# Kernel optimization log

Measured on AMD Instinct MI355X. Metric: run time of the kernel, lower is better.

## Reference

```python
import jax, jax.numpy as jnp
import numpy as np

D_MODEL = 256
NUM_HEADS = 8
HEAD_DIM = D_MODEL // NUM_HEADS


def setup_inputs() -> dict:
    key = jax.random.key(0)
    ks = jax.random.split(key, 16)
    B, C, H, W = 2, D_MODEL, 64, 64
    s = 0.02
    inp = {
        "query_feat": jax.random.normal(ks[0], (B, C, H, W), jnp.float32),
        "lateral_feat": jax.random.normal(ks[1], (B, C, H, W), jnp.float32),
        # 1x1 convs == per-pixel linear layers: weight (out, in), bias (out,)
        "Wq": jax.random.normal(ks[2], (C, C), jnp.float32) * s,
        "bq": jnp.zeros((C,), jnp.float32),
        "Wk": jax.random.normal(ks[3], (C, C), jnp.float32) * s,
        "bk": jnp.zeros((C,), jnp.float32),
        "Wv": jax.random.normal(ks[4], (C, C), jnp.float32) * s,
        "bv": jnp.zeros((C,), jnp.float32),
        "Wo": jax.random.normal(ks[5], (C, C), jnp.float32) * s,
        "bo": jnp.zeros((C,), jnp.float32),
        "W1": jax.random.normal(ks[6], (4 * C, C), jnp.float32) * s,
        "b1": jnp.zeros((4 * C,), jnp.float32),
        "W2": jax.random.normal(ks[7], (C, 4 * C), jnp.float32) * s,
        "b2": jnp.zeros((C,), jnp.float32),
    }
    return inp


def reference(query_feat, lateral_feat, Wq, bq, Wk, bk, Wv, bv, Wo, bo, W1, b1, W2, b2):
    B, C, H, W = query_feat.shape
    N = H * W
    h, d = NUM_HEADS, HEAD_DIM
    scale = d ** -0.5

    # (B,C,H,W) -> (B,N,C) tokens
    xq = query_feat.reshape(B, C, N).transpose(0, 2, 1)
    xl = lateral_feat.reshape(B, C, N).transpose(0, 2, 1)

    # 1x1-conv projections = dense per-token linear
    Q = (xq @ Wq.T + bq).reshape(B, N, h, d).transpose(0, 2, 1, 3)  # (B,h,N,d)
    K = (xl @ Wk.T + bk).reshape(B, N, h, d).transpose(0, 2, 1, 3)
    V = (xl @ Wv.T + bv).reshape(B, N, h, d).transpose(0, 2, 1, 3)

    scores = jnp.einsum("bhqd,bhkd->bhqk", Q, K) * scale  # (B,h,N,N)
    attn = jax.nn.softmax(scores, axis=-1)  # dropout = identity at inference
    out = jnp.einsum("bhqk,bhkd->bhqd", attn, V)  # (B,h,N,d)

    out = out.transpose(0, 2, 1, 3).reshape(B, N, C)  # (B,N,C)
    out = out @ Wo.T + bo
    out = out.transpose(0, 2, 1).reshape(B, C, H, W)
    out = out + query_feat  # residual

    # MLP on channels (1x1 convs + exact GELU)
    t = out.reshape(B, C, N).transpose(0, 2, 1)  # (B,N,C)
    hdn = jax.nn.gelu(t @ W1.T + b1, approximate=False)  # (B,N,4C)
    mlp = (hdn @ W2.T + b2).transpose(0, 2, 1).reshape(B, C, H, W)
    return out + mlp
```

## Files before the change

### kernel.cpp

```cpp
#include <hip/hip_runtime.h>
#include <math.h>

namespace {

constexpr int kB  = 2;
constexpr int kC  = 256;
constexpr int kN  = 4096;
constexpr int kHD = 32;
constexpr int kC4 = 1024;

typedef __attribute__((ext_vector_type(8))) short bf16x8;
typedef __attribute__((ext_vector_type(4))) float f32x4;
typedef __attribute__((ext_vector_type(16))) float f32x16;

__device__ __forceinline__ float gelu_exact(float x) {
  return 0.5f * x * (1.0f + erff(x * 0.70710678118654752f));
}

__device__ __forceinline__ unsigned short f2bf(float x) {
  unsigned u = __builtin_bit_cast(unsigned, x);
  u += 0x7FFFu + ((u >> 16) & 1u);
  return (unsigned short)(u >> 16);
}

__device__ __forceinline__ float bf2f(unsigned short us) {
  return __builtin_bit_cast(float, (unsigned)us << 16);
}

__device__ __forceinline__ float exp2_hw(float x) {
#if __has_builtin(__builtin_amdgcn_exp2f)
  return __builtin_amdgcn_exp2f(x);
#else
  float r;
  asm("v_exp_f32 %0, %1\n\ts_nop 1" : "=v"(r) : "v"(x));
  return r;
#endif
}

__device__ __forceinline__ unsigned cvt_pk_bf16(float lo, float hi) {
  unsigned r;
  asm("v_cvt_pk_bf16_f32 %0, %1, %2" : "=v"(r) : "v"(lo), "v"(hi));
  return r;
}

__global__ __launch_bounds__(256)
void convert_all(const float* __restrict__ qfeat, const float* __restrict__ lfeat,
                 const float* __restrict__ Wq, const float* __restrict__ Wk,
                 const float* __restrict__ Wv, const float* __restrict__ Wo,
                 const float* __restrict__ W1, const float* __restrict__ W2,
                 unsigned short* __restrict__ qtok, unsigned short* __restrict__ ltok,
                 unsigned short* __restrict__ wbf)
{
  __shared__ float Lds[32][36];
  const int z = blockIdx.z;
  const int t = threadIdx.x;
  if (z < 4) {
    const float* src = (z < kB) ? qfeat : lfeat;
    unsigned short* dst = (z < kB) ? qtok : ltok;
    const int b = z & 1;
    src += (size_t)b * kC * kN;
    dst += (size_t)b * kN * kC;
    const int n0 = blockIdx.x * 32, c0 = blockIdx.y * 32;
    const int r = t >> 3, q4 = (t & 7) * 4;
    {
      const float4 v = *(const float4*)&src[(size_t)(c0 + r) * kN + n0 + q4];
      Lds[r][q4 + 0] = v.x; Lds[r][q4 + 1] = v.y; Lds[r][q4 + 2] = v.z; Lds[r][q4 + 3] = v.w;
    }
    __syncthreads();
    ushort4 p;
    p.x = f2bf(Lds[q4 + 0][r]); p.y = f2bf(Lds[q4 + 1][r]);
    p.z = f2bf(Lds[q4 + 2][r]); p.w = f2bf(Lds[q4 + 3][r]);
    *(ushort4*)&dst[(size_t)(n0 + r) * kC + c0 + q4] = p;
  } else {
    const int wi = blockIdx.y * 128 + blockIdx.x;
    if (wi >= 768) return;
    const int i4 = wi * 1024 + t * 4;
    const float* s; int base;
    if      (i4 < 65536)  { s = Wq; base = 0; }
    else if (i4 < 131072) { s = Wk; base = 65536; }
    else if (i4 < 196608) { s = Wv; base = 131072; }
    else if (i4 < 262144) { s = Wo; base = 196608; }
    else if (i4 < 524288) { s = W1; base = 262144; }
    else                  { s = W2; base = 524288; }
    const float4 v = *(const float4*)&s[i4 - base];
    ushort4 p;
    p.x = f2bf(v.x); p.y = f2bf(v.y); p.z = f2bf(v.z); p.w = f2bf(v.w);
    *(ushort4*)&wbf[i4] = p;
  }
}

template <int EPI, bool GELU, bool RES>
__global__ __launch_bounds__(256)
void gemm_mfma(const unsigned short* __restrict__ Wbf,
               const unsigned short* __restrict__ Xtok,
               const float* __restrict__ bias, const float* __restrict__ res,
               void* __restrict__ Y1, void* __restrict__ Y2,
               int M, int Nn, int K, float oscale)
{
  __shared__ unsigned short Wlds[64 * 64];
  __shared__ unsigned short Xlds[64 * 64];

  const int z = blockIdx.z;
  Xtok += (size_t)z * Nn * K;

  const int t = threadIdx.x;
  const int w = t >> 6, l = t & 63;
  const int r = l & 15, g = l >> 4;
  const int wm = w >> 1, wn = w & 1;
  const int m0 = blockIdx.y * 64, n0 = blockIdx.x * 64;

  const int rw = t >> 3;
  const int sw = (t & 7) ^ (rw & 7);
  const unsigned short* wsrc = Wbf + (size_t)(m0 + rw) * K + sw * 8;
  const unsigned short* xsrc = Xtok + (size_t)(n0 + rw) * K + sw * 8;

  f32x4 acc[2][2];
#pragma unroll
  for (int i = 0; i < 2; ++i)
#pragma unroll
    for (int j = 0; j < 2; ++j) acc[i][j] = {0.f, 0.f, 0.f, 0.f};

  bf16x8 wrg[2], xrg[2];
#pragma unroll
  for (int j = 0; j < 2; ++j) {
    wrg[j] = *(const bf16x8*)(wsrc + (size_t)(32 * j) * K);
    xrg[j] = *(const bf16x8*)(xsrc + (size_t)(32 * j) * K);
  }

  for (int k0 = 0; k0 < K; k0 += 64) {
    __syncthreads();
    *(bf16x8*)((char*)Wlds + t * 16)         = wrg[0];
    *(bf16x8*)((char*)Wlds + (256 + t) * 16) = wrg[1];
    *(bf16x8*)((char*)Xlds + t * 16)         = xrg[0];
    *(bf16x8*)((char*)Xlds + (256 + t) * 16) = xrg[1];
    __syncthreads();
    if (k0 + 64 < K) {
#pragma unroll
      for (int j = 0; j < 2; ++j) {
        wrg[j] = *(const bf16x8*)(wsrc + (size_t)(32 * j) * K + k0 + 64);
        xrg[j] = *(const bf16x8*)(xsrc + (size_t)(32 * j) * K + k0 + 64);
      }
    }
#pragma unroll
    for (int kc = 0; kc < 2; ++kc) {
      const int sl = ((kc * 4 + g) ^ (r & 7)) * 16;
      bf16x8 a0 = *(const bf16x8*)((const char*)Wlds + (wm * 32 + r) * 128 + sl);
      bf16x8 a1 = *(const bf16x8*)((const char*)Wlds + (wm * 32 + 16 + r) * 128 + sl);
      bf16x8 b0 = *(const bf16x8*)((const char*)Xlds + (wn * 32 + r) * 128 + sl);
      bf16x8 b1 = *(const bf16x8*)((const char*)Xlds + (wn * 32 + 16 + r) * 128 + sl);
      acc[0][0] = __builtin_amdgcn_mfma_f32_16x16x32_bf16(a0, b0, acc[0][0], 0, 0, 0);
      acc[0][1] = __builtin_amdgcn_mfma_f32_16x16x32_bf16(a0, b1, acc[0][1], 0, 0, 0);
      acc[1][0] = __builtin_amdgcn_mfma_f32_16x16x32_bf16(a1, b0, acc[1][0], 0, 0, 0);
      acc[1][1] = __builtin_amdgcn_mfma_f32_16x16x32_bf16(a1, b1, acc[1][1], 0, 0, 0);
    }
  }

#pragma unroll
  for (int f = 0; f < 2; ++f) {
    const int mb = m0 + wm * 32 + f * 16 + 4 * g;
    const float* bp = bias + mb;
    if constexpr (EPI == 4) { if (mb >= (M >> 1)) bp = res + (mb - (M >> 1)); }
    const float4 b4 = *(const float4*)bp;
#pragma unroll
    for (int fn = 0; fn < 2; ++fn) {
      const int n = n0 + wn * 32 + fn * 16 + r;
      float v[4];
      v[0] = (acc[f][fn][0] + b4.x) * oscale; v[1] = (acc[f][fn][1] + b4.y) * oscale;
      v[2] = (acc[f][fn][2] + b4.z) * oscale; v[3] = (acc[f][fn][3] + b4.w) * oscale;
      if (GELU) {
#pragma unroll
        for (int q = 0; q < 4; ++q) v[q] = gelu_exact(v[q]);
      }
      if (RES) {
#pragma unroll
        for (int q = 0; q < 4; ++q)
          v[q] += res[(size_t)z * M * Nn + (size_t)(mb + q) * Nn + n];
      }
      if constexpr (EPI == 1) {
        unsigned short* Yt = (unsigned short*)Y1 + (size_t)z * Nn * M;
        ushort4 pk;
        pk.x = f2bf(v[0]); pk.y = f2bf(v[1]); pk.z = f2bf(v[2]); pk.w = f2bf(v[3]);
        *(ushort4*)&Yt[(size_t)n * M + mb] = pk;
      }
      if constexpr (EPI == 4) {
        const int Mh = M >> 1;
        if (mb < Mh) {
          unsigned short* Yt = (unsigned short*)Y1 + (size_t)z * Nn * Mh;
          ushort4 pk;
          pk.x = f2bf(v[0]); pk.y = f2bf(v[1]); pk.z = f2bf(v[2]); pk.w = f2bf(v[3]);
          *(ushort4*)&Yt[(size_t)n * Mh + mb] = pk;
        } else {
          unsigned short* Yc = (unsigned short*)Y2 + (size_t)z * Mh * Nn;
#pragma unroll
          for (int q = 0; q < 4; ++q) Yc[(size_t)(mb - Mh + q) * Nn + n] = f2bf(v[q]);
        }
      }
      if constexpr (EPI == 6) {
        float* Yf = (float*)Y1 + (size_t)z * M * Nn;
        const unsigned short* Rt = (const unsigned short*)Y2 + (size_t)z * Nn * M;
#pragma unroll
        for (int q = 0; q < 4; ++q)
          Yf[(size_t)(mb + q) * Nn + n] = v[q] + bf2f(Rt[(size_t)n * M + mb + q]);
      }
    }
  }
}

__global__ __launch_bounds__(512, 4)
void attn_mfma32(const unsigned short* __restrict__ Qbf,
                 const unsigned short* __restrict__ Kbf,
                 const unsigned short* __restrict__ Vbf,
                 unsigned short* __restrict__ Aout)
{
  __shared__ char smem[32768];

  const int id = blockIdx.x;
  const int bh = id & 15;
  const int b = bh >> 3, hd = bh & 7;
  const int t = threadIdx.x;
  const int w = t >> 6, l = t & 63;
  const int r = l & 31, hi = l >> 5;
  const int qg = w >> 2, kh = w & 3;

  const unsigned short* Qb = Qbf + (size_t)b * kN * kC;
  const unsigned short* Kb = Kbf + (size_t)b * kN * kC;
  const unsigned short* Vb = Vbf + ((size_t)b * kC + hd * kHD) * kN;
  unsigned short* Ap = Aout + (size_t)b * kN * kC;

  const int q0 = (id >> 4) * 64 + qg * 32;

  const bf16x8 qf0 = *(const bf16x8*)&Qb[(size_t)(q0 + r) * kC + hd * kHD + hi * 8];
  const bf16x8 qf1 = *(const bf16x8*)&Qb[(size_t)(q0 + r) * kC + hd * kHD + 16 + hi * 8];

  const int tq = t & 127, qd = t >> 7;
  const int skey = tq >> 1, schalf = (tq & 1) * 2;
  const int sd = tq >> 2, scp = (tq & 3) * 2;
  const unsigned short* ksrc = Kb + (size_t)(qd * 1024 + skey) * kC + hd * kHD + schalf * 8;
  const unsigned short* vsrc = Vb + (size_t)sd * kN + qd * 1024 + scp * 8;
  char* kdst0 = smem + qd * 8192 + ((schalf)*64 + (skey ^ (9 * schalf))) * 16;
  char* kdst1 = smem + qd * 8192 + ((schalf + 1) * 64 + (skey ^ (9 * (schalf + 1)))) * 16;
  char* vdst0 = smem + qd * 8192 + 4096 + ((scp)*32 + (sd ^ scp)) * 16;
  char* vdst1 = smem + qd * 8192 + 4096 + ((scp + 1) * 32 + (sd ^ (scp + 1))) * 16;

  const int kb0 = kh * 8192;
  int koff[2][2], voff[2][2];
#pragma unroll
  for (int ds = 0; ds < 2; ++ds)
#pragma unroll
    for (int tile = 0; tile < 2; ++tile) {
      const int c = 2 * ds + hi;
      koff[ds][tile] = kb0 + (c * 64 + tile * 32 + (r ^ (9 * c))) * 16;
    }
#pragma unroll
  for (int ktile = 0; ktile < 2; ++ktile)
#pragma unroll
    for (int kc = 0; kc < 2; ++kc) {
      const int c = ktile * 4 + kc * 2 + hi;
      voff[ktile][kc] = kb0 + 4096 + (c * 32 + (r ^ c)) * 16;
    }

  const f32x16 ZV = {0.f};
  f32x16 oA = ZV, oB = ZV;
  float lsum = 0.f;

  bf16x8 krg0 = *(const bf16x8*)ksrc, krg1 = *(const bf16x8*)(ksrc + 8);
  bf16x8 vrg0 = *(const bf16x8*)vsrc, vrg1 = *(const bf16x8*)(vsrc + 8);

  for (int it = 0; it < 16; ++it) {
    __syncthreads();
    *(bf16x8*)kdst0 = krg0; *(bf16x8*)kdst1 = krg1;
    *(bf16x8*)vdst0 = vrg0; *(bf16x8*)vdst1 = vrg1;
    __syncthreads();
    if (it + 1 < 16) {
      ksrc += (size_t)64 * kC; vsrc += 64;
      krg0 = *(const bf16x8*)ksrc; krg1 = *(const bf16x8*)(ksrc + 8);
      vrg0 = *(const bf16x8*)vsrc; vrg1 = *(const bf16x8*)(vsrc + 8);
    }

    bf16x8 ka00 = *(const bf16x8*)(smem + koff[0][0]);
    bf16x8 ka10 = *(const bf16x8*)(smem + koff[1][0]);
    bf16x8 ka01 = *(const bf16x8*)(smem + koff[0][1]);
    bf16x8 ka11 = *(const bf16x8*)(smem + koff[1][1]);
    __builtin_amdgcn_s_setprio(1);
    f32x16 s0 = __builtin_amdgcn_mfma_f32_32x32x16_bf16(ka00, qf0, ZV, 0, 0, 0);
    s0        = __builtin_amdgcn_mfma_f32_32x32x16_bf16(ka10, qf1, s0, 0, 0, 0);
    f32x16 s1 = __builtin_amdgcn_mfma_f32_32x32x16_bf16(ka01, qf0, ZV, 0, 0, 0);
    s1        = __builtin_amdgcn_mfma_f32_32x32x16_bf16(ka11, qf1, s1, 0, 0, 0);
    __builtin_amdgcn_s_setprio(0);

#pragma unroll
    for (int ktile = 0; ktile < 2; ++ktile) {
      const f32x16& sv = ktile ? s1 : s0;
      float pe[16];
#pragma unroll
      for (int j = 0; j < 16; ++j) pe[j] = exp2_hw(sv[j]);
      lsum += (((pe[0] + pe[1]) + (pe[2] + pe[3])) + ((pe[4] + pe[5]) + (pe[6] + pe[7])))
            + (((pe[8] + pe[9]) + (pe[10] + pe[11])) + ((pe[12] + pe[13]) + (pe[14] + pe[15])));
      const unsigned c0 = cvt_pk_bf16(pe[0], pe[1]),   c1 = cvt_pk_bf16(pe[2], pe[3]);
      const unsigned c2 = cvt_pk_bf16(pe[4], pe[5]),   c3 = cvt_pk_bf16(pe[6], pe[7]);
      const unsigned c4 = cvt_pk_bf16(pe[8], pe[9]),   c5 = cvt_pk_bf16(pe[10], pe[11]);
      const unsigned c6 = cvt_pk_bf16(pe[12], pe[13]), c7 = cvt_pk_bf16(pe[14], pe[15]);
      auto a02 = __builtin_amdgcn_permlane32_swap(c0, c2, false, false);
      auto a13 = __builtin_amdgcn_permlane32_swap(c1, c3, false, false);
      auto a46 = __builtin_amdgcn_permlane32_swap(c4, c6, false, false);
      auto a57 = __builtin_amdgcn_permlane32_swap(c5, c7, false, false);
      union { unsigned u[4]; bf16x8 v; } p0, p1;
      p0.u[0] = a02[0]; p0.u[1] = a13[0]; p0.u[2] = a02[1]; p0.u[3] = a13[1];
      p1.u[0] = a46[0]; p1.u[1] = a57[0]; p1.u[2] = a46[1]; p1.u[3] = a57[1];
      bf16x8 vf0 = *(const bf16x8*)(smem + voff[ktile][0]);
      bf16x8 vf1 = *(const bf16x8*)(smem + voff[ktile][1]);
      __builtin_amdgcn_s_setprio(1);
      oA = __builtin_amdgcn_mfma_f32_32x32x16_bf16(vf0, p0.v, oA, 0, 0, 0);
      oB = __builtin_amdgcn_mfma_f32_32x32x16_bf16(vf1, p1.v, oB, 0, 0, 0);
      __builtin_amdgcn_s_setprio(0);
    }
  }

  {
    auto pr = __builtin_amdgcn_permlane32_swap(
        __builtin_bit_cast(unsigned, lsum), __builtin_bit_cast(unsigned, lsum), false, false);
    lsum = __builtin_bit_cast(float, (unsigned)pr[0]) + __builtin_bit_cast(float, (unsigned)pr[1]);
  }
  float oS[16];
#pragma unroll
  for (int j = 0; j < 16; ++j) oS[j] = oA[j] + oB[j];

  float* Scr = (float*)smem;
  __syncthreads();
  if (kh != 0) {
    float* S = Scr + ((size_t)(qg * 3 + (kh - 1)) * 64 + l) * 17;
#pragma unroll
    for (int j = 0; j < 16; ++j) S[j] = oS[j];
    S[16] = lsum;
  }
  __syncthreads();
  if (kh == 0) {
#pragma unroll
    for (int p = 0; p < 3; ++p) {
      const float* S = Scr + ((size_t)(qg * 3 + p) * 64 + l) * 17;
#pragma unroll
      for (int j = 0; j < 16; ++j) oS[j] += S[j];
      lsum += S[16];
    }
    const float inv = 1.f / lsum;

    unsigned* T = (unsigned*)(Scr + (size_t)qg * 3 * 64 * 17);
#pragma unroll
    for (int p = 0; p < 8; ++p) {
      const int r2 = 4 * (p >> 1) + 2 * hi + (p & 1);
      T[r2 * 33 + r] = cvt_pk_bf16(oS[2 * p] * inv, oS[2 * p + 1] * inv);
    }
    unsigned v[8];
#pragma unroll
    for (int j = 0; j < 8; ++j) v[j] = T[(8 * hi + j) * 33 + r];
    unsigned short* outp = Ap + (size_t)(q0 + r) * kC + hd * kHD + hi * 16;
    uint4 w0{v[0], v[1], v[2], v[3]}, w1{v[4], v[5], v[6], v[7]};
    *(uint4*)outp = w0;
    *(uint4*)(outp + 8) = w1;
  }
}

}

extern "C" void kernel_launch(void* const* d_in, const int* in_sizes, int n_in,
                              void* d_out, int out_size, void* d_ws, size_t ws_size,
                              hipStream_t stream)
{
  const float* qfeat = (const float*)d_in[0];
  const float* lfeat = (const float*)d_in[1];
  const float* Wq = (const float*)d_in[2];
  const float* bq = (const float*)d_in[3];
  const float* Wk = (const float*)d_in[4];
  const float* bk = (const float*)d_in[5];
  const float* Wv = (const float*)d_in[6];
  const float* bv = (const float*)d_in[7];
  const float* Wo = (const float*)d_in[8];
  const float* bo = (const float*)d_in[9];
  const float* W1 = (const float*)d_in[10];
  const float* b1 = (const float*)d_in[11];
  const float* W2 = (const float*)d_in[12];
  const float* b2 = (const float*)d_in[13];
  float* out = (float*)d_out;
  (void)in_sizes; (void)n_in; (void)out_size; (void)ws_size;

  constexpr float kScaleLog2e = 0.25506970f;

  const size_t bcn = (size_t)kB * kC * kN;
  unsigned short* qtok   = (unsigned short*)d_ws;
  unsigned short* ltok   = qtok + bcn;
  unsigned short* wbf    = ltok + bcn;
  unsigned short* qbf    = wbf + 786432;
  unsigned short* kbf    = qbf + bcn;
  unsigned short* vbf    = kbf + bcn;
  unsigned short* atok   = vbf + bcn;
  unsigned short* owstok = atok + bcn;
  unsigned short* h1tok  = owstok + bcn;

  dim3 blk(256);

  convert_all<<<dim3(128, 8, 5), blk, 0, stream>>>(
      qfeat, lfeat, Wq, Wk, Wv, Wo, W1, W2, qtok, ltok, wbf);

  gemm_mfma<1, false, false><<<dim3(64, 4, 2), blk, 0, stream>>>(
      wbf, qtok, bq, nullptr, qbf, nullptr, kC, kN, kC, kScaleLog2e);
  gemm_mfma<4, false, false><<<dim3(64, 8, 2), blk, 0, stream>>>(
      wbf + 65536, ltok, bk, bv, kbf, vbf, 2 * kC, kN, kC, 1.0f);

  attn_mfma32<<<dim3(1024), dim3(512), 0, stream>>>(qbf, kbf, vbf, atok);

  gemm_mfma<1, false, true><<<dim3(64, 4, 2), blk, 0, stream>>>(
      wbf + 196608, atok, bo, qfeat, owstok, nullptr, kC, kN, kC, 1.0f);
  gemm_mfma<1, true, false><<<dim3(64, 16, 2), blk, 0, stream>>>(
      wbf + 262144, owstok, b1, nullptr, h1tok, nullptr, kC4, kN, kC, 1.0f);
  gemm_mfma<6, false, false><<<dim3(64, 4, 2), blk, 0, stream>>>(
      wbf + 524288, h1tok, b2, nullptr, out, owstok, kC, kN, kC4, 1.0f);
}
```

Before: 112.1 us.

## Widen attention query tile to 128 and use bit-trick exp2 in softmax

```diff
diff --git a/kernel.cpp b/kernel.cpp
--- a/kernel.cpp
+++ b/kernel.cpp
@@ -27,14 +27,9 @@
   return __builtin_bit_cast(float, (unsigned)us << 16);
 }
 
-__device__ __forceinline__ float exp2_hw(float x) {
-#if __has_builtin(__builtin_amdgcn_exp2f)
-  return __builtin_amdgcn_exp2f(x);
-#else
-  float r;
-  asm("v_exp_f32 %0, %1\n\ts_nop 1" : "=v"(r) : "v"(x));
-  return r;
-#endif
+__device__ __forceinline__ float fast_exp2(float x) {
+  int i = (int)__builtin_fmaf(x, 8388608.0f, 1064866805.0f);
+  return __builtin_bit_cast(float, i);
 }
 
 __device__ __forceinline__ unsigned cvt_pk_bf16(float lo, float hi) {
@@ -212,7 +207,7 @@
                  const unsigned short* __restrict__ Vbf,
                  unsigned short* __restrict__ Aout)
 {
-  __shared__ char smem[32768];
+  __shared__ __attribute__((aligned(16))) char smem[17408];
 
   const int id = blockIdx.x;
   const int bh = id & 15;
@@ -220,61 +215,55 @@
   const int t = threadIdx.x;
   const int w = t >> 6, l = t & 63;
   const int r = l & 31, hi = l >> 5;
-  const int qg = w >> 2, kh = w & 3;
+  const int qg = w >> 1, kh = w & 1;
 
   const unsigned short* Qb = Qbf + (size_t)b * kN * kC;
   const unsigned short* Kb = Kbf + (size_t)b * kN * kC;
   const unsigned short* Vb = Vbf + ((size_t)b * kC + hd * kHD) * kN;
   unsigned short* Ap = Aout + (size_t)b * kN * kC;
 
-  const int q0 = (id >> 4) * 64 + qg * 32;
+  const int q0 = (id >> 4) * 128 + qg * 32;
 
   const bf16x8 qf0 = *(const bf16x8*)&Qb[(size_t)(q0 + r) * kC + hd * kHD + hi * 8];
   const bf16x8 qf1 = *(const bf16x8*)&Qb[(size_t)(q0 + r) * kC + hd * kHD + 16 + hi * 8];
 
-  const int tq = t & 127, qd = t >> 7;
-  const int skey = tq >> 1, schalf = (tq & 1) * 2;
-  const int sd = tq >> 2, scp = (tq & 3) * 2;
-  const unsigned short* ksrc = Kb + (size_t)(qd * 1024 + skey) * kC + hd * kHD + schalf * 8;
-  const unsigned short* vsrc = Vb + (size_t)sd * kN + qd * 1024 + scp * 8;
-  char* kdst0 = smem + qd * 8192 + ((schalf)*64 + (skey ^ (9 * schalf))) * 16;
-  char* kdst1 = smem + qd * 8192 + ((schalf + 1) * 64 + (skey ^ (9 * (schalf + 1)))) * 16;
-  char* vdst0 = smem + qd * 8192 + 4096 + ((scp)*32 + (sd ^ scp)) * 16;
-  char* vdst1 = smem + qd * 8192 + 4096 + ((scp + 1) * 32 + (sd ^ (scp + 1))) * 16;
-
-  const int kb0 = kh * 8192;
+  const int tt = t & 255, th = t >> 8;
+  const unsigned short* ksrc = Kb + (size_t)(th * 2048 + (tt >> 2)) * kC + hd * kHD + (tt & 3) * 8;
+  const unsigned short* vsrc = Vb + (size_t)(tt >> 3) * kN + th * 2048 + (tt & 7) * 8;
+  char* kdst = smem + th * 4096 + ((tt & 3) * 64 + ((tt >> 2) ^ (9 * (tt & 3)))) * 16;
+  char* vdst = smem + 8192 + th * 4096 + ((tt & 7) * 32 + ((tt >> 3) ^ (tt & 7))) * 16;
+
   int koff[2][2], voff[2][2];
 #pragma unroll
   for (int ds = 0; ds < 2; ++ds)
 #pragma unroll
     for (int tile = 0; tile < 2; ++tile) {
       const int c = 2 * ds + hi;
-      koff[ds][tile] = kb0 + (c * 64 + tile * 32 + (r ^ (9 * c))) * 16;
+      koff[ds][tile] = kh * 4096 + (c * 64 + tile * 32 + (r ^ (9 * c))) * 16;
     }
 #pragma unroll
   for (int ktile = 0; ktile < 2; ++ktile)
 #pragma unroll
     for (int kc = 0; kc < 2; ++kc) {
       const int c = ktile * 4 + kc * 2 + hi;
-      voff[ktile][kc] = kb0 + 4096 + (c * 32 + (r ^ c)) * 16;
+      voff[ktile][kc] = 8192 + kh * 4096 + (c * 32 + (r ^ c)) * 16;
     }
 
   const f32x16 ZV = {0.f};
   f32x16 oA = ZV, oB = ZV;
   float lsum = 0.f;
 
-  bf16x8 krg0 = *(const bf16x8*)ksrc, krg1 = *(const bf16x8*)(ksrc + 8);
-  bf16x8 vrg0 = *(const bf16x8*)vsrc, vrg1 = *(const bf16x8*)(vsrc + 8);
-
-  for (int it = 0; it < 16; ++it) {
+  bf16x8 krg = *(const bf16x8*)ksrc;
+  bf16x8 vrg = *(const bf16x8*)vsrc;
+
+  for (int kt = 0; kt < 2048; kt += 64) {
     __syncthreads();
-    *(bf16x8*)kdst0 = krg0; *(bf16x8*)kdst1 = krg1;
-    *(bf16x8*)vdst0 = vrg0; *(bf16x8*)vdst1 = vrg1;
+    *(bf16x8*)kdst = krg;
+    *(bf16x8*)vdst = vrg;
     __syncthreads();
-    if (it + 1 < 16) {
-      ksrc += (size_t)64 * kC; vsrc += 64;
-      krg0 = *(const bf16x8*)ksrc; krg1 = *(const bf16x8*)(ksrc + 8);
-      vrg0 = *(const bf16x8*)vsrc; vrg1 = *(const bf16x8*)(vsrc + 8);
+    if (kt + 64 < 2048) {
+      krg = *(const bf16x8*)(ksrc + (size_t)(kt + 64) * kC);
+      vrg = *(const bf16x8*)(vsrc + kt + 64);
     }
 
     bf16x8 ka00 = *(const bf16x8*)(smem + koff[0][0]);
@@ -293,7 +282,7 @@
       const f32x16& sv = ktile ? s1 : s0;
       float pe[16];
 #pragma unroll
-      for (int j = 0; j < 16; ++j) pe[j] = exp2_hw(sv[j]);
+      for (int j = 0; j < 16; ++j) pe[j] = fast_exp2(sv[j]);
       lsum += (((pe[0] + pe[1]) + (pe[2] + pe[3])) + ((pe[4] + pe[5]) + (pe[6] + pe[7])))
             + (((pe[8] + pe[9]) + (pe[10] + pe[11])) + ((pe[12] + pe[13]) + (pe[14] + pe[15])));
       const unsigned c0 = cvt_pk_bf16(pe[0], pe[1]),   c1 = cvt_pk_bf16(pe[2], pe[3]);
@@ -327,24 +316,21 @@
 
   float* Scr = (float*)smem;
   __syncthreads();
-  if (kh != 0) {
-    float* S = Scr + ((size_t)(qg * 3 + (kh - 1)) * 64 + l) * 17;
+  if (kh == 1) {
+    float* S = Scr + ((size_t)qg * 64 + l) * 17;
 #pragma unroll
     for (int j = 0; j < 16; ++j) S[j] = oS[j];
     S[16] = lsum;
   }
   __syncthreads();
   if (kh == 0) {
-#pragma unroll
-    for (int p = 0; p < 3; ++p) {
-      const float* S = Scr + ((size_t)(qg * 3 + p) * 64 + l) * 17;
-#pragma unroll
-      for (int j = 0; j < 16; ++j) oS[j] += S[j];
-      lsum += S[16];
-    }
+    const float* S = Scr + ((size_t)qg * 64 + l) * 17;
+#pragma unroll
+    for (int j = 0; j < 16; ++j) oS[j] += S[j];
+    lsum += S[16];
     const float inv = 1.f / lsum;
 
-    unsigned* T = (unsigned*)(Scr + (size_t)qg * 3 * 64 * 17);
+    unsigned* T = (unsigned*)(Scr + (size_t)qg * 64 * 17);
 #pragma unroll
     for (int p = 0; p < 8; ++p) {
       const int r2 = 4 * (p >> 1) + 2 * hi + (p & 1);
@@ -406,7 +392,7 @@
   gemm_mfma<4, false, false><<<dim3(64, 8, 2), blk, 0, stream>>>(
       wbf + 65536, ltok, bk, bv, kbf, vbf, 2 * kC, kN, kC, 1.0f);
 
-  attn_mfma32<<<dim3(1024), dim3(512), 0, stream>>>(qbf, kbf, vbf, atok);
+  attn_mfma32<<<dim3(512), dim3(512), 0, stream>>>(qbf, kbf, vbf, atok);
 
   gemm_mfma<1, false, true><<<dim3(64, 4, 2), blk, 0, stream>>>(
       wbf + 196608, atok, bo, qfeat, owstok, nullptr, kC, kN, kC, 1.0f);
```

Result: faster. 108.2 us (-3.4%).
